# Kernel tuning notes

Hardware: AMD Instinct MI355X
Metric: run time of the kernel (lower is better)

## Reference

```python
import jax, jax.numpy as jnp
import numpy as np

MAX_POS = float(2 ** 20)  # max_position_encoding_distance
B, C, S = 2, 1536, 16384
H, T, P = 768, 367, 128
NUM_ORG = 2


def _apply_rope(x, positions):
    # x: (B, P, T, H), positions: (B, P) int -> rotate pairs (first-half, second-half)
    half = x.shape[-1] // 2
    inv_freq = 1.0 / (MAX_POS ** (jnp.arange(half, dtype=jnp.float32) / half))  # (half,)
    ang = positions.astype(jnp.float32)[:, :, None, None] * inv_freq  # (B, P, 1, half)
    cos, sin = jnp.cos(ang), jnp.sin(ang)
    x1, x2 = x[..., :half], x[..., half:]
    return jnp.concatenate([x1 * cos - x2 * sin, x1 * sin + x2 * cos], axis=-1)


def _gather_affine_rope(logits, idx, params, organism_index):
    # logits: (B, H, S); idx: (B, P); params: (ORG, 2, T, H)
    bi = jnp.arange(logits.shape[0])[:, None]
    x = logits[bi, :, idx]  # (B, P, H)
    bp = params[organism_index]  # (B, 2, T, H)
    scale = bp[:, 0][:, None]   # (B, 1, T, H)
    offset = bp[:, 1][:, None]  # (B, 1, T, H)
    x = scale * x[:, :, None, :] + offset  # (B, P, T, H)
    return _apply_rope(x, idx)


def setup_inputs() -> dict:
    key = jax.random.key(0)
    ks = jax.random.split(key, 9)
    stdv = 1.0 / np.sqrt(C)
    return {
        'embeddings_1bp': jax.random.normal(ks[0], (B, C, S), jnp.float32),
        'conv_w': jax.random.normal(ks[1], (NUM_ORG, H, C), jnp.float32) * stdv,
        'conv_b': jax.random.normal(ks[2], (NUM_ORG, H), jnp.float32) * 0.02,
        'rope_pos_donor': jax.random.normal(ks[3], (NUM_ORG, 2, T, H), jnp.float32) * 0.05,
        'rope_pos_acceptor': jax.random.normal(ks[4], (NUM_ORG, 2, T, H), jnp.float32) * 0.05,
        'rope_neg_donor': jax.random.normal(ks[5], (NUM_ORG, 2, T, H), jnp.float32) * 0.05,
        'rope_neg_acceptor': jax.random.normal(ks[6], (NUM_ORG, 2, T, H), jnp.float32) * 0.05,
        'organism_index': jax.random.randint(ks[7], (B,), 0, NUM_ORG),
        'splice_site_positions': jax.random.randint(ks[8], (B, 4, P), 0, S),
    }


def reference(embeddings_1bp, conv_w, conv_b, rope_pos_donor, rope_pos_acceptor,
              rope_neg_donor, rope_neg_acceptor, organism_index, splice_site_positions):
    pos_d, pos_a = splice_site_positions[:, 0], splice_site_positions[:, 1]
    neg_d, neg_a = splice_site_positions[:, 2], splice_site_positions[:, 3]

    # organism-indexed 1x1 conv: (B,C,S) x (B,H,C) -> (B,H,S)
    w = conv_w[organism_index]
    b = conv_b[organism_index]
    logits = jnp.einsum('bcs,boc->bos', embeddings_1bp, w) + b[:, :, None]

    pdl = _gather_affine_rope(logits, pos_d, rope_pos_donor, organism_index)
    pal = _gather_affine_rope(logits, pos_a, rope_pos_acceptor, organism_index)
    ndl = _gather_affine_rope(logits, neg_d, rope_neg_donor, organism_index)
    nal = _gather_affine_rope(logits, neg_a, rope_neg_acceptor, organism_index)

    pos_counts = jax.nn.softplus(jnp.einsum('bdth,bath->bdat', pdl, pal))  # (B,P,P,T)
    neg_counts = jax.nn.softplus(jnp.einsum('bdth,bath->bdat', ndl, nal))

    pos_mask = (pos_d >= 0)[:, :, None] & (pos_a >= 0)[:, None, :]  # (B,P,P)
    neg_mask = (neg_d >= 0)[:, :, None] & (neg_a >= 0)[:, None, :]
    # tissue_mask: default num_tracks_per_organism -> all True
    tissue_mask = jnp.ones((B, T), dtype=bool)
    pos_mask = pos_mask[:, :, :, None] & tissue_mask[:, None, None, :]
    neg_mask = neg_mask[:, :, :, None] & tissue_mask[:, None, None, :]

    junction_mask = jnp.concatenate([pos_mask, neg_mask], axis=-1)  # (B,P,P,2T)
    pred_counts = jnp.concatenate([pos_counts, neg_counts], axis=-1)
    pred_counts = jnp.where(junction_mask, pred_counts, 0.0)
    return pred_counts, junction_mask
```

## Files before the change

kernel.cpp:

```cpp
#include <hip/hip_runtime.h>
#include <hip/hip_bf16.h>
#include <math.h>
#include <string.h>

#define B_    2
#define C_    1536
#define S_    16384
#define H_    768
#define T_    367
#define P_    128
#define HALF_ 384
#define TT_   734
#define NT2_  184
#define PRED_ELEMS 24051712

#define XHH_OFF  0
#define CSH_OFF  393216
#define INVF_OFF 786432
#define XCB_OFF  787200
#define W1WS_OFF 1573632

typedef short short8 __attribute__((ext_vector_type(8)));
typedef _Float16 f16x8 __attribute__((ext_vector_type(8)));
typedef _Float16 h2    __attribute__((ext_vector_type(2)));
typedef float f32x4  __attribute__((ext_vector_type(4)));

__device__ __forceinline__ unsigned int packbf2(float a, float b) {
    __hip_bfloat162 h = __float22bfloat162_rn(make_float2(a, b));
    unsigned int r; __builtin_memcpy(&r, &h, 4); return r;
}
__device__ __forceinline__ unsigned short packbf1(float a) {
    __hip_bfloat16 h = __float2bfloat16(a);
    unsigned short r; __builtin_memcpy(&r, &h, 2); return r;
}
__device__ __forceinline__ unsigned short f2h(float x) {
    _Float16 h = (_Float16)x;
    unsigned short r; __builtin_memcpy(&r, &h, 2); return r;
}
__device__ __forceinline__ h2 bch(unsigned int v) { h2 r; __builtin_memcpy(&r, &v, 4); return r; }
__device__ __forceinline__ unsigned int hcb(h2 v) { unsigned int r; __builtin_memcpy(&r, &v, 4); return r; }

__global__ void gather_cols(const float* __restrict__ emb,
                            const int* __restrict__ sp,
                            unsigned short* __restrict__ xcb) {
    int blk = blockIdx.x;
    int p = blk & 127;
    int g = (blk >> 7) & 3;
    int b = blk >> 9;
    int s = sp[(b * 4 + g) * P_ + p];
    const float* src = emb + (size_t)b * C_ * S_ + s;
    unsigned short* dst = xcb + ((size_t)(b * 4 + g) * P_ + p) * C_;
    for (int c = threadIdx.x; c < C_; c += blockDim.x)
        dst[c] = packbf1(src[(size_t)c * S_]);
}

__global__ __launch_bounds__(256) void logits_mfma(
    const unsigned short* __restrict__ xcb, const float* __restrict__ w,
    const float* __restrict__ bias, const int* __restrict__ org,
    unsigned short* __restrict__ xhh) {
    __shared__ __align__(16) unsigned short tX[64 * 64];
    __shared__ __align__(16) unsigned short tW[64 * 64];
    int mt = blockIdx.x;
    int nt = blockIdx.y;
    int o = org[mt >> 3];
    int r0 = mt * 64, h0 = nt * 64;
    int tid = threadIdx.x;
    int lane = tid & 63, wid = tid >> 6;
    int wrow = (wid >> 1) * 32, wcol = (wid & 1) * 32;
    int lr = lane & 15, lq = lane >> 4;
    int gr0 = (lq ^ (lr & 7)) * 8;

    f32x4 acc[2][2];
    #pragma unroll
    for (int i = 0; i < 2; ++i)
        #pragma unroll
        for (int j = 0; j < 2; ++j) acc[i][j] = (f32x4){0.f, 0.f, 0.f, 0.f};

    int srow = tid >> 2, sg = tid & 3;

    for (int kc = 0; kc < C_; kc += 64) {
        if (kc) __syncthreads();
        {
            const unsigned short* src = xcb + (size_t)(r0 + srow) * C_ + kc;
            unsigned short* drow = tX + srow * 64;
            #pragma unroll
            for (int i = 0; i < 2; ++i) {
                int g = sg + i * 4;
                uint4 v = *(const uint4*)(src + g * 8);
                *(uint4*)&drow[(g ^ (srow & 7)) * 8] = v;
            }
        }
        {
            const float* srcw = w + ((size_t)o * H_ + h0 + srow) * C_ + kc;
            unsigned short* drow = tW + srow * 64;
            #pragma unroll
            for (int i = 0; i < 2; ++i) {
                int g = sg + i * 4;
                float4 v0 = *(const float4*)(srcw + g * 8);
                float4 v1 = *(const float4*)(srcw + g * 8 + 4);
                uint4 pk;
                pk.x = packbf2(v0.x, v0.y); pk.y = packbf2(v0.z, v0.w);
                pk.z = packbf2(v1.x, v1.y); pk.w = packbf2(v1.z, v1.w);
                *(uint4*)&drow[(g ^ (srow & 7)) * 8] = pk;
            }
        }
        __syncthreads();
        #pragma unroll
        for (int kk = 0; kk < 64; kk += 32) {
            short8 af[2], bf2[2];
            #pragma unroll
            for (int fi = 0; fi < 2; ++fi)
                af[fi] = *(const short8*)&tX[(wrow + fi * 16 + lr) * 64 + (gr0 ^ kk)];
            #pragma unroll
            for (int fj = 0; fj < 2; ++fj)
                bf2[fj] = *(const short8*)&tW[(wcol + fj * 16 + lr) * 64 + (gr0 ^ kk)];
            #pragma unroll
            for (int fi = 0; fi < 2; ++fi)
                #pragma unroll
                for (int fj = 0; fj < 2; ++fj)
                    acc[fi][fj] = __builtin_amdgcn_mfma_f32_16x16x32_bf16(
                        af[fi], bf2[fj], acc[fi][fj], 0, 0, 0);
        }
    }
    #pragma unroll
    for (int fi = 0; fi < 2; ++fi)
        #pragma unroll
        for (int rr = 0; rr < 4; ++rr) {
            int r = r0 + wrow + fi * 16 + lq * 4 + rr;
            #pragma unroll
            for (int fj = 0; fj < 2; ++fj) {
                int h = h0 + wcol + fj * 16 + lr;
                int hj = (h < HALF_) ? h : (h - HALF_);
                int sel = (h < HALF_) ? 0 : 1;
                xhh[(size_t)r * H_ + (hj >> 2) * 8 + sel * 4 + (hj & 3)] =
                    f2h(acc[fi][fj][rr] + bias[o * H_ + h]);
            }
        }
}

__global__ void init_invf(double* __restrict__ invf) {
    int j = threadIdx.x;
    if (j < HALF_) invf[j] = exp2(-20.0 * (double)j / 384.0);
}

__global__ void rope_table(const int* __restrict__ sp,
                           const double* __restrict__ invf,
                           unsigned short* __restrict__ csh) {
    int e = blockIdx.x * blockDim.x + threadIdx.x;
    if (e >= B_ * 4 * P_ * HALF_) return;
    int j = e % HALF_;
    int r = e / HALF_;
    int s = sp[r];
    const double TWO_PI = 6.283185307179586476925286766559;
    double ang = (double)s * invf[j];
    double k = rint(ang * (1.0 / TWO_PI));
    float fr = (float)(ang - k * TWO_PI);
    float sv, cv;
    __sincosf(fr, &sv, &cv);
    int base = r * H_ + (j >> 2) * 8 + (j & 3);
    csh[base]     = f2h(cv);
    csh[base + 4] = f2h(sv);
}

__global__ __launch_bounds__(1024, 4) void junction_mfma(
    const unsigned short* __restrict__ xhh, const unsigned short* __restrict__ csh,
    const float* __restrict__ rpd, const float* __restrict__ rpa,
    const float* __restrict__ rnd, const float* __restrict__ rna,
    const int* __restrict__ org, const int* __restrict__ sp,
    unsigned short* __restrict__ w1) {
    __shared__ __align__(16) unsigned short smem[65536];
    __shared__ __align__(16) unsigned short scofh[6144];
    __shared__ int vD[P_], vA[P_];

    int nwg = gridDim.x;
    int orig = blockIdx.x;
    int xcd = orig & 7;
    int q = nwg >> 3, r8 = nwg & 7;
    int blk = (xcd < r8 ? xcd * (q + 1) : r8 * (q + 1) + (xcd - r8) * q) + (orig >> 3);

    int tp = blk % NT2_;
    int sign = (blk / NT2_) & 1;
    int b = blk / (2 * NT2_);
    int o = org[b];
    int t0 = 2 * tp, t1 = t0 + 1;
    int t1ok = (t1 < T_);
    int t1c = t1ok ? t1 : t0;
    int gd = sign * 2, ga = sign * 2 + 1;
    const float* pd = sign ? rnd : rpd;
    const float* pa = sign ? rna : rpa;
    int tid = threadIdx.x;

    for (int e = tid; e < 6144; e += 1024) {
        int tsel = e / 3072;
        int rem = e - tsel * 3072;
        int side = rem / 1536;
        int rem2 = rem - side * 1536;
        int arr = rem2 / 768;
        int e2 = rem2 - arr * 768;
        int tt = tsel ? t1c : t0;
        const float* base = (side ? pa : pd) + ((size_t)(o * 2 + arr) * T_ + tt) * H_;
        int hj = (e2 < HALF_) ? e2 : (e2 - HALF_);
        int sel = (e2 < HALF_) ? 0 : 1;
        int pos = (hj >> 2) * 8 + sel * 4 + (hj & 3);
        scofh[((tsel * 2 + side) * 2 + arr) * 768 + pos] = f2h(base[e2]);
    }
    if (tid < P_) {
        vD[tid] = sp[(b * 4 + gd) * P_ + tid] >= 0;
        vA[tid] = sp[(b * 4 + ga) * P_ + tid] >= 0;
    }
    const unsigned short* xdh = xhh + ((size_t)(b * 4 + gd) * P_) * H_;
    const unsigned short* xah = xhh + ((size_t)(b * 4 + ga) * P_) * H_;
    const unsigned short* cdh = csh + ((size_t)(b * 4 + gd) * P_) * H_;
    const unsigned short* cah = csh + ((size_t)(b * 4 + ga) * P_) * H_;

    int lane = tid & 63, wid = tid >> 6;
    int wrow = (wid >> 2) * 32, wcol = (wid & 3) * 32;
    int lr = lane & 15, lq = lane >> 4;
    int gr0 = (lq ^ (lr & 7)) * 8;

    f32x4 a0[2][2], a1[2][2];
    #pragma unroll
    for (int i = 0; i < 2; ++i)
        #pragma unroll
        for (int j = 0; j < 2; ++j) {
            a0[i][j] = (f32x4){0.f, 0.f, 0.f, 0.f};
            a1[i][j] = (f32x4){0.f, 0.f, 0.f, 0.f};
        }

    __syncthreads();

    for (int ch = 0; ch < 12; ++ch) {
        unsigned short* bufb = smem + (ch & 1) * 32768;

        #pragma unroll
        for (int s = 0; s < 2; ++s) {
            int slot = tid + s * 1024;
            int row = slot >> 3, gran = slot & 7;
            int side = row >> 7, prow = row & 127;
            const unsigned short* xb = side ? xah : xdh;
            const unsigned short* cb = side ? cah : cdh;
            int off = prow * H_ + ch * 64 + gran * 8;
            uint4 xv = *(const uint4*)(xb + off);
            uint4 cv = *(const uint4*)(cb + off);
            int sw = prow * 64 + ((gran ^ (prow & 7)) << 3);
            int kb = (ch * 8 + gran) * 8;
            h2 cA = bch(cv.x), cB = bch(cv.y), sA = bch(cv.z), sB = bch(cv.w);
            {
                const unsigned short* cof = scofh + (side * 2) * 768;
                uint4 sc = *(const uint4*)(cof + kb);
                uint4 of = *(const uint4*)(cof + 768 + kb);
                h2 u1a = __builtin_elementwise_fma(bch(sc.x), bch(xv.x), bch(of.x));
                h2 u1b = __builtin_elementwise_fma(bch(sc.y), bch(xv.y), bch(of.y));
                h2 u2a = __builtin_elementwise_fma(bch(sc.z), bch(xv.z), bch(of.z));
                h2 u2b = __builtin_elementwise_fma(bch(sc.w), bch(xv.w), bch(of.w));
                uint4 wv;
                wv.x = hcb(__builtin_elementwise_fma(u1a, cA, -(u2a * sA)));
                wv.y = hcb(__builtin_elementwise_fma(u1b, cB, -(u2b * sB)));
                wv.z = hcb(__builtin_elementwise_fma(u1a, sA, u2a * cA));
                wv.w = hcb(__builtin_elementwise_fma(u1b, sB, u2b * cB));
                *(uint4*)&bufb[side * 8192 + sw] = wv;
            }
            {
                const unsigned short* cof = scofh + ((2 + side) * 2) * 768;
                uint4 sc = *(const uint4*)(cof + kb);
                uint4 of = *(const uint4*)(cof + 768 + kb);
                h2 u1a = __builtin_elementwise_fma(bch(sc.x), bch(xv.x), bch(of.x));
                h2 u1b = __builtin_elementwise_fma(bch(sc.y), bch(xv.y), bch(of.y));
                h2 u2a = __builtin_elementwise_fma(bch(sc.z), bch(xv.z), bch(of.z));
                h2 u2b = __builtin_elementwise_fma(bch(sc.w), bch(xv.w), bch(of.w));
                uint4 wv;
                wv.x = hcb(__builtin_elementwise_fma(u1a, cA, -(u2a * sA)));
                wv.y = hcb(__builtin_elementwise_fma(u1b, cB, -(u2b * sB)));
                wv.z = hcb(__builtin_elementwise_fma(u1a, sA, u2a * cA));
                wv.w = hcb(__builtin_elementwise_fma(u1b, sB, u2b * cB));
                *(uint4*)&bufb[16384 + side * 8192 + sw] = wv;
            }
        }
        __syncthreads();

        __builtin_amdgcn_s_setprio(1);
        {
            const unsigned short* tD = bufb;
            const unsigned short* tA = bufb + 8192;
            #pragma unroll
            for (int kk = 0; kk < 64; kk += 32) {
                f16x8 af[2], bf2[2];
                #pragma unroll
                for (int fi = 0; fi < 2; ++fi)
                    af[fi] = *(const f16x8*)&tD[(wrow + fi * 16 + lr) * 64 + (gr0 ^ kk)];
                #pragma unroll
                for (int fj = 0; fj < 2; ++fj)
                    bf2[fj] = *(const f16x8*)&tA[(wcol + fj * 16 + lr) * 64 + (gr0 ^ kk)];
                #pragma unroll
                for (int fi = 0; fi < 2; ++fi)
                    #pragma unroll
                    for (int fj = 0; fj < 2; ++fj)
                        a0[fi][fj] = __builtin_amdgcn_mfma_f32_16x16x32_f16(
                            af[fi], bf2[fj], a0[fi][fj], 0, 0, 0);
            }
        }
        {
            const unsigned short* tD = bufb + 16384;
            const unsigned short* tA = bufb + 24576;
            #pragma unroll
            for (int kk = 0; kk < 64; kk += 32) {
                f16x8 af[2], bf2[2];
                #pragma unroll
                for (int fi = 0; fi < 2; ++fi)
                    af[fi] = *(const f16x8*)&tD[(wrow + fi * 16 + lr) * 64 + (gr0 ^ kk)];
                #pragma unroll
                for (int fj = 0; fj < 2; ++fj)
                    bf2[fj] = *(const f16x8*)&tA[(wcol + fj * 16 + lr) * 64 + (gr0 ^ kk)];
                #pragma unroll
                for (int fi = 0; fi < 2; ++fi)
                    #pragma unroll
                    for (int fj = 0; fj < 2; ++fj)
                        a1[fi][fj] = __builtin_amdgcn_mfma_f32_16x16x32_f16(
                            af[fi], bf2[fj], a1[fi][fj], 0, 0, 0);
            }
        }
        __builtin_amdgcn_s_setprio(0);
    }

    #pragma unroll
    for (int fi = 0; fi < 2; ++fi) {
        #pragma unroll
        for (int rr = 0; rr < 4; ++rr) {
            int d = wrow + fi * 16 + lq * 4 + rr;
            int vd = vD[d];
            #pragma unroll
            for (int fj = 0; fj < 2; ++fj) {
                int a = wcol + fj * 16 + lr;
                int va = vA[a];
                float x0 = a0[fi][fj][rr];
                float v0 = 0.0f;
                if (vd && va) v0 = (x0 > 15.0f) ? x0 : __logf(1.0f + __expf(x0));
                smem[d * P_ + a] = packbf1(v0);
                float x1 = a1[fi][fj][rr];
                float v1 = 0.0f;
                if (vd && va) v1 = (x1 > 15.0f) ? x1 : __logf(1.0f + __expf(x1));
                smem[16384 + d * P_ + a] = packbf1(v1);
            }
        }
    }
    __syncthreads();
    const uint4* s4 = (const uint4*)smem;
    uint4* d40 = (uint4*)(w1 + (size_t)((b * 2 + sign) * T_ + t0) * (P_ * P_));
    for (int i = tid; i < 2048; i += 1024) d40[i] = s4[i];
    if (t1ok) {
        uint4* d41 = (uint4*)(w1 + (size_t)((b * 2 + sign) * T_ + t1) * (P_ * P_));
        for (int i = tid; i < 2048; i += 1024) d41[i] = s4[2048 + i];
    }
}

__global__ __launch_bounds__(256) void finalize_ws(const __hip_bfloat16* __restrict__ w1,
                                                   const int* __restrict__ sp,
                                                   float* __restrict__ pred,
                                                   float* __restrict__ mask) {
    __shared__ float tile[64 * 129];
    __shared__ float mval[P_];
    int blk = blockIdx.x;
    int tt = blk % 6;
    int d = (blk / 6) % P_;
    int bs = blk / (6 * P_);
    int b = bs >> 1, sign = bs & 1;
    int t0 = tt * 64;
    int tcnt = min(64, T_ - t0);
    int tid = threadIdx.x;

    const __hip_bfloat16* src = w1 + (size_t)bs * T_ * P_ * P_ + (size_t)d * P_;
    for (int e = tid; e < tcnt * P_; e += 256) {
        int i = e >> 7, a = e & 127;
        tile[i * 129 + a] = __bfloat162float(src[(size_t)(t0 + i) * P_ * P_ + a]);
    }
    if (tid < P_) {
        bool vd = sp[(b * 4 + sign * 2) * P_ + d] >= 0;
        bool va = sp[(b * 4 + sign * 2 + 1) * P_ + tid] >= 0;
        mval[tid] = (vd && va) ? 1.0f : 0.0f;
    }
    __syncthreads();
    size_t obase = ((size_t)(b * P_ + d) * P_) * TT_ + sign * T_ + t0;
    float* dstp = pred + obase;
    float* dstm = mask + obase;
    for (int e = tid; e < P_ * 64; e += 256) {
        int a = e >> 6, ii = e & 63;
        if (ii < tcnt) {
            dstp[(size_t)a * TT_ + ii] = tile[ii * 129 + a];
            dstm[(size_t)a * TT_ + ii] = mval[a];
        }
    }
}

__global__ __launch_bounds__(256) void transpose_out(const __hip_bfloat16* __restrict__ w1,
                                                     float* __restrict__ pred) {
    __shared__ float tile[64 * 129];
    int blk = blockIdx.x;
    int tt = blk % 6;
    int d = (blk / 6) % P_;
    int bs = blk / (6 * P_);
    int b = bs >> 1, sign = bs & 1;
    int t0 = tt * 64;
    int tcnt = min(64, T_ - t0);
    int tid = threadIdx.x;

    const __hip_bfloat16* src = w1 + (size_t)bs * T_ * P_ * P_ + (size_t)d * P_;
    for (int e = tid; e < tcnt * P_; e += 256) {
        int i = e >> 7, a = e & 127;
        tile[i * 129 + a] = __bfloat162float(src[(size_t)(t0 + i) * P_ * P_ + a]);
    }
    __syncthreads();
    float* dst = pred + ((size_t)(b * P_ + d) * P_) * TT_ + sign * T_ + t0;
    for (int e = tid; e < P_ * 64; e += 256) {
        int a = e >> 6, ii = e & 63;
        if (ii < tcnt) dst[(size_t)a * TT_ + ii] = tile[ii * 129 + a];
    }
}

__global__ void mask_fill(const int* __restrict__ sp, float* __restrict__ mask) {
    int blk = blockIdx.x;
    int a = blk & 127;
    int d = (blk >> 7) & 127;
    int b = blk >> 14;
    bool vp = (sp[(b * 4 + 0) * P_ + d] >= 0) && (sp[(b * 4 + 1) * P_ + a] >= 0);
    bool vn = (sp[(b * 4 + 2) * P_ + d] >= 0) && (sp[(b * 4 + 3) * P_ + a] >= 0);
    float* dst = mask + (size_t)blk * TT_;
    for (int st = threadIdx.x; st < TT_; st += blockDim.x)
        dst[st] = (st < T_ ? vp : vn) ? 1.0f : 0.0f;
}

extern "C" void kernel_launch(void* const* d_in, const int* in_sizes, int n_in,
                              void* d_out, int out_size, void* d_ws, size_t ws_size,
                              hipStream_t stream) {
    const float* emb  = (const float*)d_in[0];
    const float* w    = (const float*)d_in[1];
    const float* bias = (const float*)d_in[2];
    const float* rpd  = (const float*)d_in[3];
    const float* rpa  = (const float*)d_in[4];
    const float* rnd  = (const float*)d_in[5];
    const float* rna  = (const float*)d_in[6];
    const int*   org  = (const int*)d_in[7];
    const int*   sp   = (const int*)d_in[8];

    float* out = (float*)d_out;
    float* ws  = (float*)d_ws;
    unsigned short* xhh = (unsigned short*)(ws + XHH_OFF);
    unsigned short* csh = (unsigned short*)(ws + CSH_OFF);
    double* invf = (double*)(ws + INVF_OFF);
    unsigned short* xcb = (unsigned short*)(ws + XCB_OFF);
    float* pred  = out;
    float* maskp = out + PRED_ELEMS;

    size_t w1_bytes = (size_t)4 * T_ * P_ * P_ * 2;
    size_t need = (size_t)W1WS_OFF * 4 + w1_bytes;
    bool ws_ok = (ws_size >= need);
    unsigned short* w1 = ws_ok ? (unsigned short*)(ws + W1WS_OFF)
                               : (unsigned short*)maskp;

    init_invf<<<1, 384, 0, stream>>>(invf);
    gather_cols<<<1024, 256, 0, stream>>>(emb, sp, xcb);
    rope_table<<<1536, 256, 0, stream>>>(sp, invf, csh);
    dim3 gl(16, 12);
    logits_mfma<<<gl, 256, 0, stream>>>(xcb, w, bias, org, xhh);
    junction_mfma<<<2 * 2 * NT2_, 1024, 0, stream>>>(xhh, csh, rpd, rpa, rnd, rna, org, sp, w1);
    if (ws_ok) {
        finalize_ws<<<2 * 2 * P_ * 6, 256, 0, stream>>>((const __hip_bfloat16*)w1, sp, pred, maskp);
    } else {
        transpose_out<<<2 * 2 * P_ * 6, 256, 0, stream>>>((const __hip_bfloat16*)w1, pred);
        mask_fill<<<32768, 256, 0, stream>>>(sp, maskp);
    }
}
```

Measured before the change: 228.3 us.

## Split waves across two tissue tracks and prefetch next chunk into registers

The junction kernel's 16 waves are now split into two groups of eight. Each group handles one of the two tissue tracks with a 64x32 output tile, where before every wave computed both tracks with 32x32 tiles. This halves per-wave LDS traffic for the B fragments and the duplicated MFMA loop overhead. The global loads of x and cos/sin for the next K chunk are issued right after building the current chunk, overlapping their latency with the MFMA phase. Register pressure per wave is roughly unchanged (8 accumulators), but the larger A-fragment footprint may affect scheduling.

After: 230.9 us. About the same (+1.2%).

```diff
diff --git a/kernel.cpp b/kernel.cpp
--- a/kernel.cpp
+++ b/kernel.cpp
@@ -162,6 +162,22 @@
     csh[base + 4] = f2h(sv);
 }
 
+#define BUILD4(cof, xv, cAh, cBh, sAh, sBh, dst)                               \
+    {                                                                          \
+        uint4 sc = *(const uint4*)((cof) + kb);                                \
+        uint4 of = *(const uint4*)((cof) + 768 + kb);                          \
+        h2 u1a = __builtin_elementwise_fma(bch(sc.x), bch((xv).x), bch(of.x)); \
+        h2 u1b = __builtin_elementwise_fma(bch(sc.y), bch((xv).y), bch(of.y)); \
+        h2 u2a = __builtin_elementwise_fma(bch(sc.z), bch((xv).z), bch(of.z)); \
+        h2 u2b = __builtin_elementwise_fma(bch(sc.w), bch((xv).w), bch(of.w)); \
+        uint4 wv;                                                              \
+        wv.x = hcb(__builtin_elementwise_fma(u1a, (cAh), -(u2a * (sAh))));     \
+        wv.y = hcb(__builtin_elementwise_fma(u1b, (cBh), -(u2b * (sBh))));     \
+        wv.z = hcb(__builtin_elementwise_fma(u1a, (sAh), u2a * (cAh)));        \
+        wv.w = hcb(__builtin_elementwise_fma(u1b, (sBh), u2b * (cBh)));        \
+        *(uint4*)&(dst) = wv;                                                  \
+    }
+
 __global__ __launch_bounds__(1024, 4) void junction_mfma(
     const unsigned short* __restrict__ xhh, const unsigned short* __restrict__ csh,
     const float* __restrict__ rpd, const float* __restrict__ rpa,
@@ -191,18 +207,18 @@
     int tid = threadIdx.x;
 
     for (int e = tid; e < 6144; e += 1024) {
-        int tsel = e / 3072;
-        int rem = e - tsel * 3072;
+        int tsel_ = e / 3072;
+        int rem = e - tsel_ * 3072;
         int side = rem / 1536;
         int rem2 = rem - side * 1536;
         int arr = rem2 / 768;
         int e2 = rem2 - arr * 768;
-        int tt = tsel ? t1c : t0;
+        int tt = tsel_ ? t1c : t0;
         const float* base = (side ? pa : pd) + ((size_t)(o * 2 + arr) * T_ + tt) * H_;
         int hj = (e2 < HALF_) ? e2 : (e2 - HALF_);
         int sel = (e2 < HALF_) ? 0 : 1;
         int pos = (hj >> 2) * 8 + sel * 4 + (hj & 3);
-        scofh[((tsel * 2 + side) * 2 + arr) * 768 + pos] = f2h(base[e2]);
+        scofh[((tsel_ * 2 + side) * 2 + arr) * 768 + pos] = f2h(base[e2]);
     }
     if (tid < P_) {
         vD[tid] = sp[(b * 4 + gd) * P_ + tid] >= 0;
@@ -214,116 +230,81 @@
     const unsigned short* cah = csh + ((size_t)(b * 4 + ga) * P_) * H_;
 
     int lane = tid & 63, wid = tid >> 6;
-    int wrow = (wid >> 2) * 32, wcol = (wid & 3) * 32;
+    int tsel = wid >> 3;
+    int w8 = wid & 7;
+    int wrow = (w8 >> 2) * 64, wcol = (w8 & 3) * 32;
     int lr = lane & 15, lq = lane >> 4;
     int gr0 = (lq ^ (lr & 7)) * 8;
 
-    f32x4 a0[2][2], a1[2][2];
+    f32x4 acc[4][2];
     #pragma unroll
-    for (int i = 0; i < 2; ++i)
+    for (int i = 0; i < 4; ++i)
         #pragma unroll
-        for (int j = 0; j < 2; ++j) {
-            a0[i][j] = (f32x4){0.f, 0.f, 0.f, 0.f};
-            a1[i][j] = (f32x4){0.f, 0.f, 0.f, 0.f};
-        }
+        for (int j = 0; j < 2; ++j) acc[i][j] = (f32x4){0.f, 0.f, 0.f, 0.f};
+
+    int prow = tid >> 3, gran = tid & 7;
+    int sw = prow * 64 + ((gran ^ (prow & 7)) << 3);
+    const unsigned short* xd_t = xdh + prow * H_ + gran * 8;
+    const unsigned short* cd_t = cdh + prow * H_ + gran * 8;
+    const unsigned short* xa_t = xah + prow * H_ + gran * 8;
+    const unsigned short* ca_t = cah + prow * H_ + gran * 8;
+
+    uint4 pxd = *(const uint4*)xd_t;
+    uint4 pcd = *(const uint4*)cd_t;
+    uint4 pxa = *(const uint4*)xa_t;
+    uint4 pca = *(const uint4*)ca_t;
 
     __syncthreads();
 
     for (int ch = 0; ch < 12; ++ch) {
         unsigned short* bufb = smem + (ch & 1) * 32768;
-
-        #pragma unroll
-        for (int s = 0; s < 2; ++s) {
-            int slot = tid + s * 1024;
-            int row = slot >> 3, gran = slot & 7;
-            int side = row >> 7, prow = row & 127;
-            const unsigned short* xb = side ? xah : xdh;
-            const unsigned short* cb = side ? cah : cdh;
-            int off = prow * H_ + ch * 64 + gran * 8;
-            uint4 xv = *(const uint4*)(xb + off);
-            uint4 cv = *(const uint4*)(cb + off);
-            int sw = prow * 64 + ((gran ^ (prow & 7)) << 3);
-            int kb = (ch * 8 + gran) * 8;
-            h2 cA = bch(cv.x), cB = bch(cv.y), sA = bch(cv.z), sB = bch(cv.w);
-            {
-                const unsigned short* cof = scofh + (side * 2) * 768;
-                uint4 sc = *(const uint4*)(cof + kb);
-                uint4 of = *(const uint4*)(cof + 768 + kb);
-                h2 u1a = __builtin_elementwise_fma(bch(sc.x), bch(xv.x), bch(of.x));
-                h2 u1b = __builtin_elementwise_fma(bch(sc.y), bch(xv.y), bch(of.y));
-                h2 u2a = __builtin_elementwise_fma(bch(sc.z), bch(xv.z), bch(of.z));
-                h2 u2b = __builtin_elementwise_fma(bch(sc.w), bch(xv.w), bch(of.w));
-                uint4 wv;
-                wv.x = hcb(__builtin_elementwise_fma(u1a, cA, -(u2a * sA)));
-                wv.y = hcb(__builtin_elementwise_fma(u1b, cB, -(u2b * sB)));
-                wv.z = hcb(__builtin_elementwise_fma(u1a, sA, u2a * cA));
-                wv.w = hcb(__builtin_elementwise_fma(u1b, sB, u2b * cB));
-                *(uint4*)&bufb[side * 8192 + sw] = wv;
-            }
-            {
-                const unsigned short* cof = scofh + ((2 + side) * 2) * 768;
-                uint4 sc = *(const uint4*)(cof + kb);
-                uint4 of = *(const uint4*)(cof + 768 + kb);
-                h2 u1a = __builtin_elementwise_fma(bch(sc.x), bch(xv.x), bch(of.x));
-                h2 u1b = __builtin_elementwise_fma(bch(sc.y), bch(xv.y), bch(of.y));
-                h2 u2a = __builtin_elementwise_fma(bch(sc.z), bch(xv.z), bch(of.z));
-                h2 u2b = __builtin_elementwise_fma(bch(sc.w), bch(xv.w), bch(of.w));
-                uint4 wv;
-                wv.x = hcb(__builtin_elementwise_fma(u1a, cA, -(u2a * sA)));
-                wv.y = hcb(__builtin_elementwise_fma(u1b, cB, -(u2b * sB)));
-                wv.z = hcb(__builtin_elementwise_fma(u1a, sA, u2a * cA));
-                wv.w = hcb(__builtin_elementwise_fma(u1b, sB, u2b * cB));
-                *(uint4*)&bufb[16384 + side * 8192 + sw] = wv;
-            }
+        int kb = (ch * 8 + gran) * 8;
+
+        {
+            h2 cA = bch(pcd.x), cB = bch(pcd.y), sA = bch(pcd.z), sB = bch(pcd.w);
+            BUILD4(scofh,        pxd, cA, cB, sA, sB, bufb[sw]);
+            BUILD4(scofh + 3072, pxd, cA, cB, sA, sB, bufb[16384 + sw]);
+        }
+        {
+            h2 cA = bch(pca.x), cB = bch(pca.y), sA = bch(pca.z), sB = bch(pca.w);
+            BUILD4(scofh + 1536, pxa, cA, cB, sA, sB, bufb[8192 + sw]);
+            BUILD4(scofh + 4608, pxa, cA, cB, sA, sB, bufb[24576 + sw]);
+        }
+        if (ch < 11) {
+            int o2 = (ch + 1) * 64;
+            pxd = *(const uint4*)(xd_t + o2);
+            pcd = *(const uint4*)(cd_t + o2);
+            pxa = *(const uint4*)(xa_t + o2);
+            pca = *(const uint4*)(ca_t + o2);
         }
         __syncthreads();
 
         __builtin_amdgcn_s_setprio(1);
         {
-            const unsigned short* tD = bufb;
-            const unsigned short* tA = bufb + 8192;
+            const unsigned short* tD = bufb + tsel * 16384;
+            const unsigned short* tA = tD + 8192;
             #pragma unroll
             for (int kk = 0; kk < 64; kk += 32) {
-                f16x8 af[2], bf2[2];
+                f16x8 af[4], bf2[2];
                 #pragma unroll
-                for (int fi = 0; fi < 2; ++fi)
+                for (int fi = 0; fi < 4; ++fi)
                     af[fi] = *(const f16x8*)&tD[(wrow + fi * 16 + lr) * 64 + (gr0 ^ kk)];
                 #pragma unroll
                 for (int fj = 0; fj < 2; ++fj)
                     bf2[fj] = *(const f16x8*)&tA[(wcol + fj * 16 + lr) * 64 + (gr0 ^ kk)];
                 #pragma unroll
-                for (int fi = 0; fi < 2; ++fi)
+                for (int fi = 0; fi < 4; ++fi)
                     #pragma unroll
                     for (int fj = 0; fj < 2; ++fj)
-                        a0[fi][fj] = __builtin_amdgcn_mfma_f32_16x16x32_f16(
-                            af[fi], bf2[fj], a0[fi][fj], 0, 0, 0);
+                        acc[fi][fj] = __builtin_amdgcn_mfma_f32_16x16x32_f16(
+                            af[fi], bf2[fj], acc[fi][fj], 0, 0, 0);
             }
         }
-        {
-            const unsigned short* tD = bufb + 16384;
-            const unsigned short* tA = bufb + 24576;
-            #pragma unroll
-            for (int kk = 0; kk < 64; kk += 32) {
-                f16x8 af[2], bf2[2];
-                #pragma unroll
-                for (int fi = 0; fi < 2; ++fi)
-                    af[fi] = *(const f16x8*)&tD[(wrow + fi * 16 + lr) * 64 + (gr0 ^ kk)];
-                #pragma unroll
-                for (int fj = 0; fj < 2; ++fj)
-                    bf2[fj] = *(const f16x8*)&tA[(wcol + fj * 16 + lr) * 64 + (gr0 ^ kk)];
-                #pragma unroll
-                for (int fi = 0; fi < 2; ++fi)
-                    #pragma unroll
-                    for (int fj = 0; fj < 2; ++fj)
-                        a1[fi][fj] = __builtin_amdgcn_mfma_f32_16x16x32_f16(
-                            af[fi], bf2[fj], a1[fi][fj], 0, 0, 0);
-            }
-        }
         __builtin_amdgcn_s_setprio(0);
     }
 
     #pragma unroll
-    for (int fi = 0; fi < 2; ++fi) {
+    for (int fi = 0; fi < 4; ++fi) {
         #pragma unroll
         for (int rr = 0; rr < 4; ++rr) {
             int d = wrow + fi * 16 + lq * 4 + rr;
@@ -331,15 +312,10 @@
             #pragma unroll
             for (int fj = 0; fj < 2; ++fj) {
                 int a = wcol + fj * 16 + lr;
-                int va = vA[a];
-                float x0 = a0[fi][fj][rr];
-                float v0 = 0.0f;
-                if (vd && va) v0 = (x0 > 15.0f) ? x0 : __logf(1.0f + __expf(x0));
-                smem[d * P_ + a] = packbf1(v0);
-                float x1 = a1[fi][fj][rr];
-                float v1 = 0.0f;
-                if (vd && va) v1 = (x1 > 15.0f) ? x1 : __logf(1.0f + __expf(x1));
-                smem[16384 + d * P_ + a] = packbf1(v1);
+                float x = acc[fi][fj][rr];
+                float v = 0.0f;
+                if (vd && vA[a]) v = (x > 15.0f) ? x : __logf(1.0f + __expf(x));
+                smem[tsel * 16384 + d * P_ + a] = packbf1(v);
             }
         }
     }
```
